# Performance work log

Measured on AMD Instinct MI355X. Metric: run time of the kernel, lower is better.

## Reference

```python
import jax, jax.numpy as jnp
import numpy as np

B, T, N, F_IN, GH, LH, NC = 64, 256, 61, 3, 64, 128, 10

# NOTE: dropout layers are identity here (eval-mode semantics), as in model.eval().
# F.gelu in torch is the exact (erf) gelu -> approximate=False.

def setup_inputs() -> dict:
    key = jax.random.key(0)
    ks = jax.random.split(key, 24)
    s = lambda k, shp: jax.random.normal(k, shp, jnp.float32) * 0.05
    return {
        "x": jax.random.normal(ks[0], (B, T, N * F_IN), jnp.float32),
        "adj": jax.random.uniform(ks[1], (N, N), jnp.float32) / N,
        "W_g1": s(ks[2], (GH, F_IN)), "b_g1": s(ks[3], (GH,)),
        "W_g2": s(ks[4], (GH, GH)), "b_g2": s(ks[5], (GH,)),
        "Wih_l0": s(ks[6], (2, 4 * LH, N * GH)), "Whh_l0": s(ks[7], (2, 4 * LH, LH)),
        "bih_l0": s(ks[8], (2, 4 * LH)), "bhh_l0": s(ks[9], (2, 4 * LH)),
        "Wih_l1": s(ks[10], (2, 4 * LH, 2 * LH)), "Whh_l1": s(ks[11], (2, 4 * LH, LH)),
        "bih_l1": s(ks[12], (2, 4 * LH)), "bhh_l1": s(ks[13], (2, 4 * LH)),
        "Wa1": s(ks[14], (64, 2 * LH)), "ba1": s(ks[15], (64,)),
        "Wa2": s(ks[16], (1, 64)), "ba2": s(ks[17], (1,)),
        "Wc1": s(ks[18], (LH, 2 * LH)), "bc1": s(ks[19], (LH,)),
        "Wc2": s(ks[20], (NC, LH)), "bc2": s(ks[21], (NC,)),
    }


def _lstm_layer(inp, Wih, Whh, bih, bhh):
    # inp: [B, T, D]; Wih: [2, 4H, D]; Whh: [2, 4H, H]; gate order i,f,g,o (torch)
    outs = []
    for d in range(2):
        pre = jnp.einsum('btd,gd->btg', inp, Wih[d]) + bih[d] + bhh[d]  # [B,T,4H]
        pre_t = jnp.swapaxes(pre, 0, 1)  # [T,B,4H]
        if d == 1:
            pre_t = pre_t[::-1]
        Whh_d = Whh[d]

        def step(carry, p):
            h, c = carry
            g = p + h @ Whh_d.T
            i, f, gc, o = jnp.split(g, 4, axis=-1)
            c = jax.nn.sigmoid(f) * c + jax.nn.sigmoid(i) * jnp.tanh(gc)
            h = jax.nn.sigmoid(o) * jnp.tanh(c)
            return (h, c), h

        h0 = jnp.zeros((inp.shape[0], Whh_d.shape[-1]), inp.dtype)
        _, ys = jax.lax.scan(step, (h0, h0), pre_t)
        if d == 1:
            ys = ys[::-1]
        outs.append(jnp.swapaxes(ys, 0, 1))  # [B,T,H]
    return jnp.concatenate(outs, axis=-1)  # [B,T,2H]


def reference(x, adj, W_g1, b_g1, W_g2, b_g2,
              Wih_l0, Whh_l0, bih_l0, bhh_l0,
              Wih_l1, Whh_l1, bih_l1, bhh_l1,
              Wa1, ba1, Wa2, ba2, Wc1, bc1, Wc2, bc2):
    b, t, _ = x.shape
    h = x.reshape(b, t, N, F_IN)
    # GCN layer 1: adjacency propagate + 1x1 conv (linear over feature dim) + gelu
    h = jnp.einsum('nm,btmf->btnf', adj, h)
    h = jax.nn.gelu(h @ W_g1.T + b_g1, approximate=False)
    # GCN layer 2
    h = jnp.einsum('nm,btmf->btnf', adj, h)
    h = jax.nn.gelu(h @ W_g2.T + b_g2, approximate=False)
    seq = h.reshape(b, t, N * GH)  # [B,T,3904]
    l0 = _lstm_layer(seq, Wih_l0, Whh_l0, bih_l0, bhh_l0)
    l1 = _lstm_layer(l0, Wih_l1, Whh_l1, bih_l1, bhh_l1)  # [B,T,2H]
    # attention pooling
    scores = (jnp.tanh(l1 @ Wa1.T + ba1) @ Wa2.T + ba2).squeeze(-1)  # [B,T]
    w = jax.nn.softmax(scores, axis=1)[..., None]
    ctx = jnp.sum(l1 * w, axis=1)  # [B,2H]
    hid = jax.nn.relu(ctx @ Wc1.T + bc1)
    return hid @ Wc2.T + bc2  # [B,NC]
```

## Files before the change

### kernel.cpp

```cpp
#include <hip/hip_runtime.h>
#include <math.h>

#define B_    64
#define T_    256
#define N_    61
#define FIN_  3
#define GH_   64
#define LH_   128
#define NC_   10
#define NG_   3904
#define M_TOT 16384
#define CHUNK_M 8192
#define SUB_M   2048

typedef __attribute__((ext_vector_type(8))) short bf16x8;
typedef __attribute__((ext_vector_type(4))) float f32x4;

__device__ __forceinline__ float gelu_exact(float x) {
    return 0.5f * x * (1.0f + erff(x * 0.70710678118654752f));
}
__device__ __forceinline__ float sigmoidf_(float x) {
    return 1.0f / (1.0f + expf(-x));
}
__device__ __forceinline__ unsigned short f2bf(float f) {
    unsigned int u = __float_as_uint(f);
    u = (u + 0x7FFFu + ((u >> 16) & 1u)) >> 16;
    return (unsigned short)u;
}
__device__ __forceinline__ void store_h(float* p, float v) { *p = v; }
__device__ __forceinline__ void store_h(unsigned short* p, float v) { *p = f2bf(v); }

__device__ __forceinline__ void gload_lds16(const void* g, void* l) {
    __builtin_amdgcn_global_load_lds(
        (const __attribute__((address_space(1))) unsigned int*)g,
        (__attribute__((address_space(3))) unsigned int*)l,
        16, 0, 0);
}

__device__ __forceinline__ int swz(int row, int k) { return k ^ ((row & 3) << 4); }

__global__ __launch_bounds__(256) void cvt_bf16_kernel(
    const float* __restrict__ in, unsigned short* __restrict__ out, int n4)
{
    int i = blockIdx.x * 256 + threadIdx.x;
    if (i < n4) {
        float4 v = reinterpret_cast<const float4*>(in)[i];
        ushort4 o;
        o.x = f2bf(v.x); o.y = f2bf(v.y); o.z = f2bf(v.z); o.w = f2bf(v.w);
        reinterpret_cast<ushort4*>(out)[i] = o;
    }
}

__global__ __launch_bounds__(256) void cvt_adj_kernel(
    const float* __restrict__ adj, unsigned short* __restrict__ adjb)
{
    int i = blockIdx.x * 256 + threadIdx.x;
    if (i < 4096) {
        int n = i >> 6, m = i & 63;
        unsigned short v = (n < N_ && m < N_) ? f2bf(adj[n * N_ + m]) : (unsigned short)0;
        adjb[n * 64 + swz(n, m)] = v;
    }
}

__global__ __launch_bounds__(256) void cvt_w2_kernel(
    const float* __restrict__ W2, unsigned short* __restrict__ w2b)
{
    int i = blockIdx.x * 256 + threadIdx.x;
    if (i < 4096) {
        int c = i >> 6, f = i & 63;
        w2b[c * 64 + swz(c, f)] = f2bf(W2[c * 64 + f]);
    }
}

__global__ __launch_bounds__(256) void gcn_h1_kernel(
    const float* __restrict__ x, const float* __restrict__ adj,
    const float* __restrict__ W1, const float* __restrict__ b1,
    unsigned short* __restrict__ H1W, int bt_base)
{
    __shared__ float adjs[N_ * 65];
    __shared__ float h1s [N_ * 65];
    __shared__ float xs [184];
    __shared__ float axs[184];
    __shared__ float w1s[192];
    __shared__ float b1s[64];

    const int tid = threadIdx.x;
    const int bt  = bt_base + blockIdx.x;

    for (int i = tid; i < N_ * N_; i += 256) {
        int n = i / 61, m = i - n * 61;
        adjs[n * 65 + m] = adj[i];
    }
    for (int i = tid; i < N_ * FIN_; i += 256) xs[i] = x[(size_t)bt * (N_ * FIN_) + i];
    for (int i = tid; i < GH_ * FIN_; i += 256) w1s[i] = W1[i];
    if (tid < GH_) b1s[tid] = b1[tid];
    __syncthreads();

    if (tid < N_ * FIN_) {
        int n = tid / 3, f = tid - n * 3;
        float acc = 0.f;
        for (int m = 0; m < N_; ++m) acc += adjs[n * 65 + m] * xs[m * 3 + f];
        axs[tid] = acc;
    }
    __syncthreads();

    for (int u = 0; u < 16; ++u) {
        int idx = tid + u * 256;
        if (idx < N_ * GH_) {
            int m = idx >> 6, c = idx & 63;
            float acc = b1s[c];
            acc += axs[m * 3 + 0] * w1s[c * 3 + 0];
            acc += axs[m * 3 + 1] * w1s[c * 3 + 1];
            acc += axs[m * 3 + 2] * w1s[c * 3 + 2];
            h1s[m * 65 + c] = gelu_exact(acc);
        }
    }
    __syncthreads();

    unsigned short* dst = H1W + (size_t)blockIdx.x * 4096;
    for (int i = tid; i < 4096; i += 256) {
        int c = i >> 6, m = i & 63;
        unsigned short v = (m < N_) ? f2bf(h1s[m * 65 + c]) : (unsigned short)0;
        dst[c * 64 + swz(c, m)] = v;
    }
}

__global__ __launch_bounds__(256) void gcn_mix_kernel(
    const unsigned short* __restrict__ H1W,
    const unsigned short* __restrict__ adjb,
    const unsigned short* __restrict__ w2b,
    const float* __restrict__ b2,
    unsigned short* __restrict__ seqc,
    int sc_base)
{
    __shared__ unsigned short adjbs[64 * 64];
    __shared__ unsigned short b1t [128 * 64];
    __shared__ unsigned short w2bs[64 * 64];
    __shared__ unsigned short T   [128 * 64];
    __shared__ float b2s[64];

    const int tid = threadIdx.x;
    const int w   = tid >> 6;
    const int l   = tid & 63;
    const int lr  = l & 15, lk = l >> 4;
    const int p   = blockIdx.x;

    #pragma unroll
    for (int q = 0; q < 2; ++q)
        gload_lds16(adjb + q * 2048 + w * 512 + l * 8, &adjbs[q * 2048 + w * 512]);
    #pragma unroll
    for (int q = 0; q < 2; ++q)
        gload_lds16(w2b + q * 2048 + w * 512 + l * 8, &w2bs[q * 2048 + w * 512]);
    #pragma unroll
    for (int q = 0; q < 4; ++q)
        gload_lds16(H1W + (size_t)p * 8192 + q * 2048 + w * 512 + l * 8,
                    &b1t[q * 2048 + w * 512]);
    if (tid < 64) b2s[tid] = b2[tid];
    __syncthreads();

    f32x4 acc1[4][2];
    #pragma unroll
    for (int i = 0; i < 4; ++i)
        #pragma unroll
        for (int j = 0; j < 2; ++j) acc1[i][j] = (f32x4){0.f, 0.f, 0.f, 0.f};

    #pragma unroll
    for (int kk = 0; kk < 2; ++kk) {
        const int kb = kk * 32 + lk * 8;
        bf16x8 af[4], bfr[2];
        #pragma unroll
        for (int i = 0; i < 4; ++i) {
            int rn = i * 16 + lr;
            af[i] = *reinterpret_cast<const bf16x8*>(&adjbs[rn * 64 + swz(rn, kb)]);
        }
        #pragma unroll
        for (int j = 0; j < 2; ++j) {
            int rb = w * 32 + j * 16 + lr;
            bfr[j] = *reinterpret_cast<const bf16x8*>(&b1t[rb * 64 + swz(rb, kb)]);
        }
        #pragma unroll
        for (int i = 0; i < 4; ++i)
            #pragma unroll
            for (int j = 0; j < 2; ++j)
                acc1[i][j] = __builtin_amdgcn_mfma_f32_16x16x32_bf16(af[i], bfr[j], acc1[i][j], 0, 0, 0);
    }

    #pragma unroll
    for (int i = 0; i < 4; ++i) {
        #pragma unroll
        for (int j = 0; j < 2; ++j) {
            int col = w * 32 + j * 16 + lr;
            int c   = col & 63;
            int rbase = (col >> 6) * 64;
            #pragma unroll
            for (int r = 0; r < 4; ++r) {
                int n   = i * 16 + lk * 4 + r;
                int row = rbase + n;
                T[row * 64 + swz(row, c)] = f2bf(acc1[i][j][r]);
            }
        }
    }
    __syncthreads();

    f32x4 acc2[2][4];
    #pragma unroll
    for (int i = 0; i < 2; ++i)
        #pragma unroll
        for (int j = 0; j < 4; ++j) acc2[i][j] = (f32x4){0.f, 0.f, 0.f, 0.f};

    #pragma unroll
    for (int kk = 0; kk < 2; ++kk) {
        const int kb = kk * 32 + lk * 8;
        bf16x8 a2[2], bw[4];
        #pragma unroll
        for (int i = 0; i < 2; ++i) {
            int r2 = w * 32 + i * 16 + lr;
            a2[i] = *reinterpret_cast<const bf16x8*>(&T[r2 * 64 + swz(r2, kb)]);
        }
        #pragma unroll
        for (int j = 0; j < 4; ++j) {
            int co = j * 16 + lr;
            bw[j] = *reinterpret_cast<const bf16x8*>(&w2bs[co * 64 + swz(co, kb)]);
        }
        #pragma unroll
        for (int i = 0; i < 2; ++i)
            #pragma unroll
            for (int j = 0; j < 4; ++j)
                acc2[i][j] = __builtin_amdgcn_mfma_f32_16x16x32_bf16(a2[i], bw[j], acc2[i][j], 0, 0, 0);
    }

    #pragma unroll
    for (int i = 0; i < 2; ++i) {
        #pragma unroll
        for (int j = 0; j < 4; ++j) {
            int co = j * 16 + lr;
            float bias = b2s[co];
            #pragma unroll
            for (int r = 0; r < 4; ++r) {
                int row = w * 32 + i * 16 + lk * 4 + r;
                int n   = row & 63;
                if (n < N_) {
                    int btc = sc_base + p * 2 + (row >> 6);
                    seqc[(size_t)btc * NG_ + n * 64 + co] =
                        f2bf(gelu_exact(acc2[i][j][r] + bias));
                }
            }
        }
    }
}

__global__ __launch_bounds__(256) void gemm_mfma_kernel(
    const unsigned short* __restrict__ A, const unsigned short* __restrict__ W,
    const float* __restrict__ bias_a, const float* __restrict__ bias_b,
    float* __restrict__ Cout, int K, int m_base, int Mtot)
{
    __shared__ unsigned short As[128 * 32];
    __shared__ unsigned short Bs[128 * 32];

    const int tid = threadIdx.x;
    const int w   = tid >> 6;
    const int l   = tid & 63;
    const int wr  = w >> 1, wc = w & 1;
    const int lr  = l & 15, lk = l >> 4;

    const int m0 = blockIdx.x * 128;
    const int n0 = blockIdx.y * 128;

    f32x4 acc[4][4];
    #pragma unroll
    for (int i = 0; i < 4; ++i)
        #pragma unroll
        for (int j = 0; j < 4; ++j) acc[i][j] = (f32x4){0.f, 0.f, 0.f, 0.f};

    const int row_a0 = tid >> 2;
    const int cb     = (tid & 3) * 8;
    const unsigned short* aptr0 = A + (size_t)(m0 + row_a0) * K + cb;
    const unsigned short* aptr1 = A + (size_t)(m0 + row_a0 + 64) * K + cb;
    const unsigned short* bptr0 = W + (size_t)(n0 + row_a0) * K + cb;
    const unsigned short* bptr1 = W + (size_t)(n0 + row_a0 + 64) * K + cb;
    unsigned short* lA0 = &As[w * 512];
    unsigned short* lA1 = &As[2048 + w * 512];
    unsigned short* lB0 = &Bs[w * 512];
    unsigned short* lB1 = &Bs[2048 + w * 512];

    for (int k0 = 0; k0 < K; k0 += 32) {
        gload_lds16(aptr0 + k0, lA0);
        gload_lds16(aptr1 + k0, lA1);
        gload_lds16(bptr0 + k0, lB0);
        gload_lds16(bptr1 + k0, lB1);
        __syncthreads();

        bf16x8 af[4], bfr[4];
        #pragma unroll
        for (int i = 0; i < 4; ++i)
            af[i] = *reinterpret_cast<const bf16x8*>(&As[(wr * 64 + i * 16 + lr) * 32 + lk * 8]);
        #pragma unroll
        for (int j = 0; j < 4; ++j)
            bfr[j] = *reinterpret_cast<const bf16x8*>(&Bs[(wc * 64 + j * 16 + lr) * 32 + lk * 8]);
        #pragma unroll
        for (int i = 0; i < 4; ++i)
            #pragma unroll
            for (int j = 0; j < 4; ++j)
                acc[i][j] = __builtin_amdgcn_mfma_f32_16x16x32_bf16(af[i], bfr[j], acc[i][j], 0, 0, 0);
        __syncthreads();
    }

    #pragma unroll
    for (int i = 0; i < 4; ++i) {
        #pragma unroll
        for (int j = 0; j < 4; ++j) {
            int n = n0 + wc * 64 + j * 16 + lr;
            float ba = bias_a[n] + bias_b[n];
            int d = n >> 9, g = n & 511;
            #pragma unroll
            for (int r = 0; r < 4; ++r) {
                int m = m_base + m0 + wr * 64 + i * 16 + lk * 4 + r;
                Cout[((size_t)d * Mtot + m) * 512 + g] = acc[i][j][r] + ba;
            }
        }
    }
}

template <typename OT>
__global__ __launch_bounds__(1024) void lstm_kernel(
    const float* __restrict__ pre,
    const float* __restrict__ Whh,
    OT* __restrict__ hout)
{
    const int d   = blockIdx.x >> 6;
    const int b   = blockIdx.x & 63;
    const int tid = threadIdx.x;
    const int g   = tid & 511;
    const int kh  = tid >> 9;

    float w[64];
    const float* wsrc = Whh + ((size_t)d * 512 + g) * 128 + kh * 64;
    #pragma unroll
    for (int k = 0; k < 64; ++k) w[k] = wsrc[k];

    __shared__ __align__(16) float h_lds[128];
    __shared__ float part[1024];
    __shared__ float gates[512];

    if (tid < 128) h_lds[tid] = 0.f;
    float c = 0.f;
    __syncthreads();

    const float* prebase = pre + ((size_t)(d * B_ + b)) * T_ * 512;

    for (int s = 0; s < T_; ++s) {
        int t = d ? (T_ - 1 - s) : s;
        float p = (tid < 512) ? prebase[(size_t)t * 512 + g] : 0.f;

        float acc0 = 0.f, acc1 = 0.f;
        #pragma unroll
        for (int k4 = 0; k4 < 16; ++k4) {
            float4 hv = *reinterpret_cast<const float4*>(&h_lds[kh * 64 + k4 * 4]);
            acc0 += w[k4 * 4 + 0] * hv.x; acc1 += w[k4 * 4 + 1] * hv.y;
            acc0 += w[k4 * 4 + 2] * hv.z; acc1 += w[k4 * 4 + 3] * hv.w;
        }
        part[tid] = acc0 + acc1;
        __syncthreads();
        if (tid < 512) gates[g] = p + part[g] + part[g + 512];
        __syncthreads();
        if (tid < 128) {
            float gi = gates[tid], gf = gates[tid + 128];
            float gc = gates[tid + 256], go = gates[tid + 384];
            c = sigmoidf_(gf) * c + sigmoidf_(gi) * tanhf(gc);
            float h = sigmoidf_(go) * tanhf(c);
            h_lds[tid] = h;
            store_h(&hout[((size_t)b * T_ + t) * 256 + d * 128 + tid], h);
        }
        __syncthreads();
    }
}

__global__ __launch_bounds__(256) void attn_scores_kernel(
    const float* __restrict__ l1, const float* __restrict__ Wa1,
    const float* __restrict__ ba1, const float* __restrict__ Wa2,
    const float* __restrict__ ba2, float* __restrict__ scores)
{
    const int b   = blockIdx.x;
    const int t0  = blockIdx.y * 32;
    const int tid = threadIdx.x;
    const int j   = tid & 63, kq = tid >> 6;

    float w[64];
    const float* wsrc = Wa1 + j * 256 + kq * 64;
    #pragma unroll
    for (int k = 0; k < 64; ++k) w[k] = wsrc[k];

    __shared__ __align__(16) float rows[32 * 256];
    __shared__ float part[256];

    const float4* src = reinterpret_cast<const float4*>(
        l1 + (size_t)b * T_ * 256 + (size_t)t0 * 256);
    float4* dstv = reinterpret_cast<float4*>(rows);
    #pragma unroll
    for (int q = 0; q < 8; ++q) dstv[q * 256 + tid] = src[q * 256 + tid];

    float wa2 = (tid < 64) ? Wa2[tid] : 0.f;
    float bj  = (tid < 64) ? ba1[tid] : 0.f;
    float bb2 = ba2[0];
    __syncthreads();

    for (int tl = 0; tl < 32; ++tl) {
        const float* row = &rows[tl * 256 + kq * 64];
        float acc = 0.f;
        #pragma unroll
        for (int k4 = 0; k4 < 16; ++k4) {
            float4 hv = *reinterpret_cast<const float4*>(&row[k4 * 4]);
            acc += w[k4 * 4 + 0] * hv.x + w[k4 * 4 + 1] * hv.y
                 + w[k4 * 4 + 2] * hv.z + w[k4 * 4 + 3] * hv.w;
        }
        part[tid] = acc;
        __syncthreads();
        if (tid < 64) {
            float dj = part[tid] + part[tid + 64] + part[tid + 128] + part[tid + 192];
            float sv = tanhf(dj + bj) * wa2;
            #pragma unroll
            for (int off = 32; off > 0; off >>= 1) sv += __shfl_xor(sv, off);
            if (tid == 0) scores[b * T_ + t0 + tl] = sv + bb2;
        }
        __syncthreads();
    }
}

__global__ __launch_bounds__(256) void attn_head_kernel(
    const float* __restrict__ l1, const float* __restrict__ scores,
    const float* __restrict__ Wc1, const float* __restrict__ bc1,
    const float* __restrict__ Wc2, const float* __restrict__ bc2,
    float* __restrict__ out)
{
    const int b   = blockIdx.x;
    const int tid = threadIdx.x;
    __shared__ float wsl[256];
    __shared__ float red[8];
    __shared__ float ctx[256];
    __shared__ float hid[128];
    __shared__ float wc1s[128 * 65];

    float v = scores[b * T_ + tid];
    float mx = v;
    #pragma unroll
    for (int off = 32; off > 0; off >>= 1) mx = fmaxf(mx, __shfl_xor(mx, off));
    if ((tid & 63) == 0) red[tid >> 6] = mx;
    __syncthreads();
    mx = fmaxf(fmaxf(red[0], red[1]), fmaxf(red[2], red[3]));
    float e = expf(v - mx);
    float s = e;
    #pragma unroll
    for (int off = 32; off > 0; off >>= 1) s += __shfl_xor(s, off);
    if ((tid & 63) == 0) red[4 + (tid >> 6)] = s;
    __syncthreads();
    float denom = red[4] + red[5] + red[6] + red[7];
    wsl[tid] = e / denom;
    __syncthreads();

    float acc = 0.f;
    const float* lb = l1 + (size_t)b * T_ * 256 + tid;
    #pragma unroll 4
    for (int t = 0; t < T_; ++t) acc += lb[(size_t)t * 256] * wsl[t];
    ctx[tid] = acc;
    __syncthreads();

    float hacc = (tid < 128) ? bc1[tid] : 0.f;
    for (int kb = 0; kb < 4; ++kb) {
        for (int i = tid; i < 128 * 64; i += 256) {
            int jj = i >> 6, kk = i & 63;
            wc1s[jj * 65 + kk] = Wc1[jj * 256 + kb * 64 + kk];
        }
        __syncthreads();
        if (tid < 128) {
            #pragma unroll
            for (int kk = 0; kk < 64; ++kk)
                hacc += ctx[kb * 64 + kk] * wc1s[tid * 65 + kk];
        }
        __syncthreads();
    }
    if (tid < 128) hid[tid] = fmaxf(hacc, 0.f);
    __syncthreads();

    if (tid < NC_) {
        float a = bc2[tid];
        #pragma unroll
        for (int k = 0; k < 128; ++k) a += hid[k] * Wc2[tid * 128 + k];
        out[b * NC_ + tid] = a;
    }
}

extern "C" void kernel_launch(void* const* d_in, const int* in_sizes, int n_in,
                              void* d_out, int out_size, void* d_ws, size_t ws_size,
                              hipStream_t stream)
{
    const float* x    = (const float*)d_in[0];
    const float* adj  = (const float*)d_in[1];
    const float* Wg1  = (const float*)d_in[2];
    const float* bg1  = (const float*)d_in[3];
    const float* Wg2  = (const float*)d_in[4];
    const float* bg2  = (const float*)d_in[5];
    const float* Wih0 = (const float*)d_in[6];
    const float* Whh0 = (const float*)d_in[7];
    const float* bih0 = (const float*)d_in[8];
    const float* bhh0 = (const float*)d_in[9];
    const float* Wih1 = (const float*)d_in[10];
    const float* Whh1 = (const float*)d_in[11];
    const float* bih1 = (const float*)d_in[12];
    const float* bhh1 = (const float*)d_in[13];
    const float* Wa1  = (const float*)d_in[14];
    const float* ba1  = (const float*)d_in[15];
    const float* Wa2  = (const float*)d_in[16];
    const float* ba2  = (const float*)d_in[17];
    const float* Wc1  = (const float*)d_in[18];
    const float* bc1  = (const float*)d_in[19];
    const float* Wc2  = (const float*)d_in[20];
    const float* bc2  = (const float*)d_in[21];

    char* ws = (char*)d_ws;
    unsigned short* seqb = (unsigned short*)(ws);
    unsigned short* l0b  = (unsigned short*)(ws);
    float*          l1f  = (float*)(ws + 8388608);
    float*          scr  = (float*)(ws + 25165824);
    unsigned short* H1W  = (unsigned short*)(ws + 64000000);
    unsigned short* adjb = (unsigned short*)(ws + 80777216);
    unsigned short* w2b  = (unsigned short*)(ws + 80785408);
    float*          pre  = (float*)(ws + 80793600);
    unsigned short* W0b  = (unsigned short*)(ws + 147902464);
    unsigned short* W1b  = (unsigned short*)(ws + 155897856);

    const int n0e = in_sizes[6];
    const int n1e = in_sizes[10];
    cvt_bf16_kernel<<<(n0e / 4 + 255) / 256, 256, 0, stream>>>(Wih0, W0b, n0e / 4);
    cvt_bf16_kernel<<<(n1e / 4 + 255) / 256, 256, 0, stream>>>(Wih1, W1b, n1e / 4);
    cvt_adj_kernel<<<16, 256, 0, stream>>>(adj, adjb);
    cvt_w2_kernel <<<16, 256, 0, stream>>>(Wg2, w2b);

    for (int ch = 0; ch < 2; ++ch) {
        int m_base = ch * CHUNK_M;
        for (int sc = 0; sc < CHUNK_M / SUB_M; ++sc) {
            gcn_h1_kernel<<<SUB_M, 256, 0, stream>>>(
                x, adj, Wg1, bg1, H1W, m_base + sc * SUB_M);
            gcn_mix_kernel<<<SUB_M / 2, 256, 0, stream>>>(
                H1W, adjb, w2b, bg2, seqb, sc * SUB_M);
        }
        gemm_mfma_kernel<<<dim3(CHUNK_M / 128, 8), 256, 0, stream>>>(
            seqb, W0b, bih0, bhh0, pre, NG_, m_base, M_TOT);
    }
    lstm_kernel<<<128, 1024, 0, stream>>>(pre, Whh0, l0b);
    gemm_mfma_kernel<<<dim3(M_TOT / 128, 8), 256, 0, stream>>>(
        l0b, W1b, bih1, bhh1, pre, 256, 0, M_TOT);
    lstm_kernel<<<128, 1024, 0, stream>>>(pre, Whh1, l1f);
    attn_scores_kernel<<<dim3(B_, 8), 256, 0, stream>>>(l1f, Wa1, ba1, Wa2, ba2, scr);
    attn_head_kernel<<<B_, 256, 0, stream>>>(l1f, scr, Wc1, bc1, Wc2, bc2, (float*)d_out);
}
```

Measured before the change: 1.085 ms.

## Restructure LSTM recurrence with shuffle-based gate reduction and double-buffered hidden state

Remaps threads in the LSTM recurrence so that the two K-halves and the four gates of each hidden unit sit in adjacent lanes of one wavefront. The partial sums and gate values are then combined with warp shuffles instead of through shared-memory part/gates arrays. The hidden state is double-buffered so each timestep needs one barrier instead of three. The next timestep's preactivation is prefetched a step ahead. The catch is that the gate math now runs on only one lane in eight, and global reads of pre become strided across lanes.

Result: slower. 1.395 ms (+28.6%).

```diff
diff --git a/kernel.cpp b/kernel.cpp
--- a/kernel.cpp
+++ b/kernel.cpp
@@ -327,50 +327,56 @@
     const float* __restrict__ Whh,
     OT* __restrict__ hout)
 {
-    const int d   = blockIdx.x >> 6;
-    const int b   = blockIdx.x & 63;
-    const int tid = threadIdx.x;
-    const int g   = tid & 511;
-    const int kh  = tid >> 9;
+    const int d    = blockIdx.x >> 6;
+    const int b    = blockIdx.x & 63;
+    const int tid  = threadIdx.x;
+    const int u    = tid >> 3;
+    const int gate = (tid >> 1) & 3;
+    const int kh   = tid & 1;
+    const int gidx = gate * 128 + u;
 
     float w[64];
-    const float* wsrc = Whh + ((size_t)d * 512 + g) * 128 + kh * 64;
+    const float* wsrc = Whh + ((size_t)d * 512 + gidx) * 128 + kh * 64;
     #pragma unroll
     for (int k = 0; k < 64; ++k) w[k] = wsrc[k];
 
-    __shared__ __align__(16) float h_lds[128];
-    __shared__ float part[1024];
-    __shared__ float gates[512];
-
-    if (tid < 128) h_lds[tid] = 0.f;
+    __shared__ __align__(16) float hbuf[2][128];
+    if (tid < 128) hbuf[0][tid] = 0.f;
     float c = 0.f;
     __syncthreads();
 
-    const float* prebase = pre + ((size_t)(d * B_ + b)) * T_ * 512;
+    const float* prebase = pre + ((size_t)(d * B_ + b)) * T_ * 512 + gidx;
+
+    float p = (kh == 0) ? prebase[(size_t)(d ? T_ - 1 : 0) * 512] : 0.f;
 
     for (int s = 0; s < T_; ++s) {
-        int t = d ? (T_ - 1 - s) : s;
-        float p = (tid < 512) ? prebase[(size_t)t * 512 + g] : 0.f;
-
-        float acc0 = 0.f, acc1 = 0.f;
+        const int t = d ? (T_ - 1 - s) : s;
+
+        float p_next = 0.f;
+        if (kh == 0 && s + 1 < T_) {
+            int tn = d ? (T_ - 2 - s) : (s + 1);
+            p_next = prebase[(size_t)tn * 512];
+        }
+
+        const float* hprev = hbuf[s & 1];
+        float acc = p;
         #pragma unroll
         for (int k4 = 0; k4 < 16; ++k4) {
-            float4 hv = *reinterpret_cast<const float4*>(&h_lds[kh * 64 + k4 * 4]);
-            acc0 += w[k4 * 4 + 0] * hv.x; acc1 += w[k4 * 4 + 1] * hv.y;
-            acc0 += w[k4 * 4 + 2] * hv.z; acc1 += w[k4 * 4 + 3] * hv.w;
-        }
-        part[tid] = acc0 + acc1;
-        __syncthreads();
-        if (tid < 512) gates[g] = p + part[g] + part[g + 512];
-        __syncthreads();
-        if (tid < 128) {
-            float gi = gates[tid], gf = gates[tid + 128];
-            float gc = gates[tid + 256], go = gates[tid + 384];
-            c = sigmoidf_(gf) * c + sigmoidf_(gi) * tanhf(gc);
-            float h = sigmoidf_(go) * tanhf(c);
-            h_lds[tid] = h;
-            store_h(&hout[((size_t)b * T_ + t) * 256 + d * 128 + tid], h);
-        }
+            float4 hv = *reinterpret_cast<const float4*>(&hprev[kh * 64 + k4 * 4]);
+            acc += w[k4 * 4 + 0] * hv.x + w[k4 * 4 + 1] * hv.y
+                 + w[k4 * 4 + 2] * hv.z + w[k4 * 4 + 3] * hv.w;
+        }
+        float sum = acc + __shfl_xor(acc, 1);
+        float sf  = __shfl_down(sum, 2);
+        float sgc = __shfl_down(sum, 4);
+        float so  = __shfl_down(sum, 6);
+        if ((tid & 7) == 0) {
+            c = sigmoidf_(sf) * c + sigmoidf_(sum) * tanhf(sgc);
+            float h = sigmoidf_(so) * tanhf(c);
+            hbuf[(s + 1) & 1][u] = h;
+            store_h(&hout[((size_t)b * T_ + t) * 256 + d * 128 + u], h);
+        }
+        p = p_next;
         __syncthreads();
     }
 }
```

## Prefetch LSTM gate preactivations two steps ahead and batch hidden-state stores

Applied to the files above, without the earlier changes.

The LSTM recurrence kernel drops the intermediate gates array and one barrier per step, so the 128 cell threads sum partial dot products straight from the part buffer. Gate preactivations are loaded from global memory by those same threads two timesteps ahead in registers, which hides load latency behind the serial recurrence. Hidden outputs go to an 8-slot LDS stage and are written out by all 1024 threads every 8 steps instead of by 128 threads each step. The cost is more registers per thread in a kernel that already holds 64 weights, and the gate sum is now done by 128 threads rather than 512.

Result: no change. 1.102 ms (+1.6%).

```diff
diff --git a/kernel.cpp b/kernel.cpp
--- a/kernel.cpp
+++ b/kernel.cpp
@@ -340,17 +340,31 @@
 
     __shared__ __align__(16) float h_lds[128];
     __shared__ float part[1024];
-    __shared__ float gates[512];
+    __shared__ float hstage[8][128];
 
     if (tid < 128) h_lds[tid] = 0.f;
     float c = 0.f;
-    __syncthreads();
-
-    const float* prebase = pre + ((size_t)(d * B_ + b)) * T_ * 512;
+
+    const float* pb = pre + ((size_t)(d * B_ + b)) * T_ * 512 + (tid & 127);
+    float pA0 = 0.f, pA1 = 0.f, pA2 = 0.f, pA3 = 0.f;
+    float pB0 = 0.f, pB1 = 0.f, pB2 = 0.f, pB3 = 0.f;
+    if (tid < 128) {
+        size_t o0 = (size_t)(d ? T_ - 1 : 0) * 512;
+        size_t o1 = (size_t)(d ? T_ - 2 : 1) * 512;
+        pA0 = pb[o0];       pA1 = pb[o0 + 128];
+        pA2 = pb[o0 + 256]; pA3 = pb[o0 + 384];
+        pB0 = pb[o1];       pB1 = pb[o1 + 128];
+        pB2 = pb[o1 + 256]; pB3 = pb[o1 + 384];
+    }
+    __syncthreads();
 
     for (int s = 0; s < T_; ++s) {
-        int t = d ? (T_ - 1 - s) : s;
-        float p = (tid < 512) ? prebase[(size_t)t * 512 + g] : 0.f;
+        float pC0 = 0.f, pC1 = 0.f, pC2 = 0.f, pC3 = 0.f;
+        if (tid < 128 && s + 2 < T_) {
+            size_t on = (size_t)(d ? T_ - 3 - s : s + 2) * 512;
+            pC0 = pb[on];       pC1 = pb[on + 128];
+            pC2 = pb[on + 256]; pC3 = pb[on + 384];
+        }
 
         float acc0 = 0.f, acc1 = 0.f;
         #pragma unroll
@@ -361,17 +375,28 @@
         }
         part[tid] = acc0 + acc1;
         __syncthreads();
-        if (tid < 512) gates[g] = p + part[g] + part[g + 512];
-        __syncthreads();
+
         if (tid < 128) {
-            float gi = gates[tid], gf = gates[tid + 128];
-            float gc = gates[tid + 256], go = gates[tid + 384];
-            c = sigmoidf_(gf) * c + sigmoidf_(gi) * tanhf(gc);
+            float gi = pA0 + part[tid]       + part[tid + 512];
+            float gf = pA1 + part[tid + 128] + part[tid + 640];
+            float gv = pA2 + part[tid + 256] + part[tid + 768];
+            float go = pA3 + part[tid + 384] + part[tid + 896];
+            c = sigmoidf_(gf) * c + sigmoidf_(gi) * tanhf(gv);
             float h = sigmoidf_(go) * tanhf(c);
             h_lds[tid] = h;
-            store_h(&hout[((size_t)b * T_ + t) * 256 + d * 128 + tid], h);
-        }
-        __syncthreads();
+            hstage[s & 7][tid] = h;
+        }
+        pA0 = pB0; pA1 = pB1; pA2 = pB2; pA3 = pB3;
+        pB0 = pC0; pB1 = pC1; pB2 = pC2; pB3 = pC3;
+        __syncthreads();
+
+        if ((s & 7) == 7) {
+            int slot = tid >> 7;
+            int u    = tid & 127;
+            int ss   = s - 7 + slot;
+            int tt   = d ? (T_ - 1 - ss) : ss;
+            store_h(&hout[((size_t)b * T_ + tt) * 256 + d * 128 + u], hstage[slot][u]);
+        }
     }
 }
 
```

## Run LSTM recurrence with bf16 MFMA over 16-batch tiles and prefetched gates

Applied to the files above, without the earlier changes.

Rewrites the LSTM recurrent kernel so that each 512-thread block handles 16 batch rows for one direction. The h·Whh product runs as bf16 MFMA with Whh held in registers, and h is double-buffered in swizzled LDS with one barrier per step. The precomputed gate inputs are prefetched two timesteps ahead. This cuts per-step synchronisation and scalar FMA work, but drops the grid from 128 blocks to 8, converts the recurrent weights and hidden state to bf16 (adding precision error), and needs an extra weight conversion pass.

Result: slower. 1.747 ms (+61.1%).

```diff
diff --git a/kernel.cpp b/kernel.cpp
--- a/kernel.cpp
+++ b/kernel.cpp
@@ -39,6 +39,8 @@
 
 __device__ __forceinline__ int swz(int row, int k) { return k ^ ((row & 3) << 4); }
 
+__device__ __forceinline__ int hswz(int row, int byteoff) { return byteoff ^ ((row & 7) << 4); }
+
 __global__ __launch_bounds__(256) void cvt_bf16_kernel(
     const float* __restrict__ in, unsigned short* __restrict__ out, int n4)
 {
@@ -322,56 +324,100 @@
 }
 
 template <typename OT>
-__global__ __launch_bounds__(1024) void lstm_kernel(
+__global__ __launch_bounds__(512) void lstm_kernel(
     const float* __restrict__ pre,
-    const float* __restrict__ Whh,
+    const unsigned short* __restrict__ Whb,
     OT* __restrict__ hout)
 {
-    const int d   = blockIdx.x >> 6;
-    const int b   = blockIdx.x & 63;
+    const int d   = blockIdx.x >> 2;
+    const int bg  = blockIdx.x & 3;
     const int tid = threadIdx.x;
-    const int g   = tid & 511;
-    const int kh  = tid >> 9;
-
-    float w[64];
-    const float* wsrc = Whh + ((size_t)d * 512 + g) * 128 + kh * 64;
-    #pragma unroll
-    for (int k = 0; k < 64; ++k) w[k] = wsrc[k];
-
-    __shared__ __align__(16) float h_lds[128];
-    __shared__ float part[1024];
-    __shared__ float gates[512];
-
-    if (tid < 128) h_lds[tid] = 0.f;
-    float c = 0.f;
-    __syncthreads();
-
-    const float* prebase = pre + ((size_t)(d * B_ + b)) * T_ * 512;
-
+    const int w   = tid >> 6;
+    const int l   = tid & 63;
+    const int lr  = l & 15;
+    const int lk  = l >> 4;
+    const int unit = w * 16 + lr;
+
+    bf16x8 bw[4][4];
+    #pragma unroll
+    for (int g = 0; g < 4; ++g)
+        #pragma unroll
+        for (int kt = 0; kt < 4; ++kt)
+            bw[g][kt] = *reinterpret_cast<const bf16x8*>(
+                Whb + ((size_t)d * 512 + g * 128 + unit) * 128 + kt * 32 + lk * 8);
+
+    __shared__ unsigned short hbuf[2][16 * 128];
+    for (int i = tid; i < 1024; i += 512)
+        reinterpret_cast<unsigned int*>(&hbuf[0][0])[i] = 0u;
+
+    float cst[4] = {0.f, 0.f, 0.f, 0.f};
+
+    const float* pb = pre + ((size_t)(d * B_ + bg * 16) * T_) * 512 + unit;
+
+    f32x4 pA[4], pB[4], pC[4];
+    {
+        int t0 = d ? (T_ - 1) : 0;
+        int t1 = d ? (T_ - 2) : 1;
+        #pragma unroll
+        for (int g = 0; g < 4; ++g)
+            #pragma unroll
+            for (int r = 0; r < 4; ++r) {
+                pA[g][r] = pb[((size_t)(lk * 4 + r) * T_ + t0) * 512 + g * 128];
+                pB[g][r] = pb[((size_t)(lk * 4 + r) * T_ + t1) * 512 + g * 128];
+            }
+    }
+    __syncthreads();
+
+    int cur = 0;
     for (int s = 0; s < T_; ++s) {
-        int t = d ? (T_ - 1 - s) : s;
-        float p = (tid < 512) ? prebase[(size_t)t * 512 + g] : 0.f;
-
-        float acc0 = 0.f, acc1 = 0.f;
-        #pragma unroll
-        for (int k4 = 0; k4 < 16; ++k4) {
-            float4 hv = *reinterpret_cast<const float4*>(&h_lds[kh * 64 + k4 * 4]);
-            acc0 += w[k4 * 4 + 0] * hv.x; acc1 += w[k4 * 4 + 1] * hv.y;
-            acc0 += w[k4 * 4 + 2] * hv.z; acc1 += w[k4 * 4 + 3] * hv.w;
-        }
-        part[tid] = acc0 + acc1;
-        __syncthreads();
-        if (tid < 512) gates[g] = p + part[g] + part[g + 512];
-        __syncthreads();
-        if (tid < 128) {
-            float gi = gates[tid], gf = gates[tid + 128];
-            float gc = gates[tid + 256], go = gates[tid + 384];
-            c = sigmoidf_(gf) * c + sigmoidf_(gi) * tanhf(gc);
-            float h = sigmoidf_(go) * tanhf(c);
-            h_lds[tid] = h;
-            store_h(&hout[((size_t)b * T_ + t) * 256 + d * 128 + tid], h);
-        }
-        __syncthreads();
+        const int t = d ? (T_ - 1 - s) : s;
+
+        const char* hb = (const char*)&hbuf[cur][0];
+        const int rowb = lr * 256;
+        const int xo   = (lr & 7) << 4;
+        bf16x8 a0 = *reinterpret_cast<const bf16x8*>(hb + rowb + ((0 * 64 + lk * 16) ^ xo));
+        bf16x8 a1 = *reinterpret_cast<const bf16x8*>(hb + rowb + ((1 * 64 + lk * 16) ^ xo));
+        bf16x8 a2 = *reinterpret_cast<const bf16x8*>(hb + rowb + ((2 * 64 + lk * 16) ^ xo));
+        bf16x8 a3 = *reinterpret_cast<const bf16x8*>(hb + rowb + ((3 * 64 + lk * 16) ^ xo));
+
+        if (s + 2 < T_) {
+            int tn = d ? (T_ - 3 - s) : (s + 2);
+            #pragma unroll
+            for (int g = 0; g < 4; ++g)
+                #pragma unroll
+                for (int r = 0; r < 4; ++r)
+                    pC[g][r] = pb[((size_t)(lk * 4 + r) * T_ + tn) * 512 + g * 128];
+        }
+
+        f32x4 acc[4];
+        #pragma unroll
+        for (int g = 0; g < 4; ++g) acc[g] = pA[g];
+        #pragma unroll
+        for (int g = 0; g < 4; ++g) {
+            acc[g] = __builtin_amdgcn_mfma_f32_16x16x32_bf16(a0, bw[g][0], acc[g], 0, 0, 0);
+            acc[g] = __builtin_amdgcn_mfma_f32_16x16x32_bf16(a1, bw[g][1], acc[g], 0, 0, 0);
+            acc[g] = __builtin_amdgcn_mfma_f32_16x16x32_bf16(a2, bw[g][2], acc[g], 0, 0, 0);
+            acc[g] = __builtin_amdgcn_mfma_f32_16x16x32_bf16(a3, bw[g][3], acc[g], 0, 0, 0);
+        }
+
+        char* hn = (char*)&hbuf[cur ^ 1][0];
+        #pragma unroll
+        for (int r = 0; r < 4; ++r) {
+            float gi = acc[0][r], gf = acc[1][r], gv = acc[2][r], go = acc[3][r];
+            cst[r] = sigmoidf_(gf) * cst[r] + sigmoidf_(gi) * tanhf(gv);
+            float h = sigmoidf_(go) * tanhf(cst[r]);
+            int m = lk * 4 + r;
+            *(unsigned short*)(hn + m * 256 + hswz(m, unit * 2)) = f2bf(h);
+            store_h(&hout[((size_t)(bg * 16 + m) * T_ + t) * 256 + d * 128 + unit], h);
+        }
+
+        #pragma unroll
+        for (int g = 0; g < 4; ++g) { pA[g] = pB[g]; pB[g] = pC[g]; }
+
+        asm volatile("s_waitcnt lgkmcnt(0)" ::: "memory");
+        __builtin_amdgcn_s_barrier();
+        __builtin_amdgcn_sched_barrier(0);
+        cur ^= 1;
     }
 }
 
@@ -527,11 +573,17 @@
     float*          pre  = (float*)(ws + 80793600);
     unsigned short* W0b  = (unsigned short*)(ws + 147902464);
     unsigned short* W1b  = (unsigned short*)(ws + 155897856);
+    unsigned short* W0hb = (unsigned short*)(ws + 156422144);
+    unsigned short* W1hb = (unsigned short*)(ws + 156684288);
 
     const int n0e = in_sizes[6];
     const int n1e = in_sizes[10];
+    const int h0e = in_sizes[7];
+    const int h1e = in_sizes[11];
     cvt_bf16_kernel<<<(n0e / 4 + 255) / 256, 256, 0, stream>>>(Wih0, W0b, n0e / 4);
     cvt_bf16_kernel<<<(n1e / 4 + 255) / 256, 256, 0, stream>>>(Wih1, W1b, n1e / 4);
+    cvt_bf16_kernel<<<(h0e / 4 + 255) / 256, 256, 0, stream>>>(Whh0, W0hb, h0e / 4);
+    cvt_bf16_kernel<<<(h1e / 4 + 255) / 256, 256, 0, stream>>>(Whh1, W1hb, h1e / 4);
     cvt_adj_kernel<<<16, 256, 0, stream>>>(adj, adjb);
     cvt_w2_kernel <<<16, 256, 0, stream>>>(Wg2, w2b);
 
@@ -546,10 +598,10 @@
         gemm_mfma_kernel<<<dim3(CHUNK_M / 128, 8), 256, 0, stream>>>(
             seqb, W0b, bih0, bhh0, pre, NG_, m_base, M_TOT);
     }
-    lstm_kernel<<<128, 1024, 0, stream>>>(pre, Whh0, l0b);
+    lstm_kernel<<<8, 512, 0, stream>>>(pre, W0hb, l0b);
     gemm_mfma_kernel<<<dim3(M_TOT / 128, 8), 256, 0, stream>>>(
         l0b, W1b, bih1, bhh1, pre, 256, 0, M_TOT);
-    lstm_kernel<<<128, 1024, 0, stream>>>(pre, Whh1, l1f);
+    lstm_kernel<<<8, 512, 0, stream>>>(pre, W1hb, l1f);
     attn_scores_kernel<<<dim3(B_, 8), 256, 0, stream>>>(l1f, Wa1, ba1, Wa2, ba2, scr);
     attn_head_kernel<<<B_, 256, 0, stream>>>(l1f, scr, Wc1, bc1, Wc2, bc2, (float*)d_out);
 }
```
